# Optimization experiments

Hardware: AMD Instinct MI355X
Metric: run time of the kernel (lower is better)

## Reference

```python
import jax, jax.numpy as jnp
import numpy as np

P = 4; PSIZE = 16; EPS = 1e-8; LAM = 1e-3; MF = 2.0; ITERS = 2
BATCH = 64; A = 64; B = 8; C = 16; D = 16; E = 10


def _conv2d(x, w, b, stride, pad):
    y = jax.lax.conv_general_dilated(x, w, (stride, stride), [(pad, pad), (pad, pad)],
                                     dimension_numbers=('NCHW', 'OIHW', 'NCHW'))
    return y + b[None, :, None, None]


def _patches(x, K, stride):
    # x: (b, H, W, F) -> (b, oh, ow, K, K, F) sliding KxK windows with given stride
    b, H, W, F = x.shape
    oh = (H - K) // stride + 1
    ow = (W - K) // stride + 1
    ih = jnp.arange(oh) * stride
    iw = jnp.arange(ow) * stride
    p = x[:, ih[:, None] + jnp.arange(K)[None, :]]          # (b, oh, K, W, F)
    p = p[:, :, :, iw[:, None] + jnp.arange(K)[None, :]]    # (b, oh, K, ow, K, F)
    return p.transpose(0, 1, 3, 2, 4, 5), oh, ow


def _fuzzy_routing(v, a_in, beta_u, beta_a):
    # Fuzzy (c-means style) routing. v: (n, N, Cout, PSIZE) votes, a_in: (n, N).
    n, N, Cc, _ = v.shape
    r = jnp.full((n, N, Cc), 1.0 / Cc, dtype=v.dtype)
    aw = a_in[:, :, None]
    for t in range(ITERS):
        rm = (r ** MF) * aw                                             # fuzzified, activation-weighted
        coeff = rm / (jnp.sum(rm, axis=1, keepdims=True) + EPS)         # (n, N, C)
        mu = jnp.einsum('bnc,bncp->bcp', coeff, v)                      # (n, C, PSIZE)
        if t < ITERS - 1:
            dist = jnp.sum((v - mu[:, None]) ** 2, axis=-1) + EPS       # (n, N, C)
            inv = dist ** (-1.0 / (MF - 1.0))
            r = inv / (jnp.sum(inv, axis=2, keepdims=True) + EPS)
    sigma_sq = jnp.einsum('bnc,bncp->bcp', coeff, (v - mu[:, None]) ** 2) + EPS
    r_sum = jnp.sum((r ** MF) * aw, axis=1)                             # (n, C)
    cost = (beta_u[None, :, None] + 0.5 * jnp.log(sigma_sq)) * r_sum[:, :, None]
    a_out = jax.nn.sigmoid(LAM * (beta_a[None, :] - jnp.sum(cost, axis=2)))
    return mu, a_out


def _conv_caps(pose, a, W, beta_u, beta_a, K, stride):
    # pose: (b, H, W, Bi, PSIZE), a: (b, H, W, Bi); W: (K*K*Bi, Co, P, P)
    b, H, Wd, Bi, _ = pose.shape
    Co = W.shape[1]
    pp, oh, ow = _patches(pose.reshape(b, H, Wd, Bi * PSIZE), K, stride)
    ap, _, _ = _patches(a, K, stride)
    n = b * oh * ow
    pp = pp.reshape(n, K * K * Bi, P, P)
    ap = ap.reshape(n, K * K * Bi)
    v = jnp.einsum('nipq,icqr->nicpr', pp, W).reshape(n, K * K * Bi, Co, PSIZE)
    mu, a_out = _fuzzy_routing(v, ap, beta_u, beta_a)
    return mu.reshape(b, oh, ow, Co, PSIZE), a_out.reshape(b, oh, ow, Co)


def _class_caps(pose, a, W, beta_u, beta_a):
    # K=1, weight-shared over positions, with coordinate addition.
    b, H, Wd, Bi, _ = pose.shape
    Co = W.shape[1]
    v = jnp.einsum('bhwipq,icqr->bhwicpr', pose.reshape(b, H, Wd, Bi, P, P), W)
    v = v.reshape(b, H, Wd, Bi, Co, PSIZE)
    ch = (jnp.arange(H, dtype=v.dtype) / H)[None, :, None, None, None]
    cw = (jnp.arange(Wd, dtype=v.dtype) / Wd)[None, None, :, None, None]
    v = v.at[..., 0].add(ch)
    v = v.at[..., 1].add(cw)
    v = v.reshape(b, H * Wd * Bi, Co, PSIZE)
    return _fuzzy_routing(v, a.reshape(b, -1), beta_u, beta_a)


def setup_inputs():
    key = jax.random.key(0)
    ks = jax.random.split(key, 8)
    return {
        'x': jax.random.normal(ks[0], (BATCH, 1, 32, 32), jnp.float32),
        'conv1_w': jax.random.normal(ks[1], (A, 1, 5, 5), jnp.float32) * 0.1,
        'conv1_b': jnp.zeros((A,), jnp.float32),
        'bn_g': jnp.ones((A,), jnp.float32),
        'bn_b': jnp.zeros((A,), jnp.float32),
        'bn_mean': jnp.zeros((A,), jnp.float32),
        'bn_var': jnp.ones((A,), jnp.float32),
        'prim_pose_w': jax.random.normal(ks[2], (B * PSIZE, A, 1, 1), jnp.float32) * 0.1,
        'prim_pose_b': jnp.zeros((B * PSIZE,), jnp.float32),
        'prim_a_w': jax.random.normal(ks[3], (B, A, 1, 1), jnp.float32) * 0.1,
        'prim_a_b': jnp.zeros((B,), jnp.float32),
        'w1': jax.random.normal(ks[4], (3 * 3 * B, C, P, P), jnp.float32),
        'bu1': jnp.zeros((C,), jnp.float32),
        'ba1': jnp.zeros((C,), jnp.float32),
        'w2': jax.random.normal(ks[5], (3 * 3 * C, D, P, P), jnp.float32),
        'bu2': jnp.zeros((D,), jnp.float32),
        'ba2': jnp.zeros((D,), jnp.float32),
        'wc': jax.random.normal(ks[6], (D, E, P, P), jnp.float32),
        'buc': jnp.zeros((E,), jnp.float32),
        'bac': jnp.zeros((E,), jnp.float32),
    }


def reference(x, conv1_w, conv1_b, bn_g, bn_b, bn_mean, bn_var,
              prim_pose_w, prim_pose_b, prim_a_w, prim_a_b,
              w1, bu1, ba1, w2, bu2, ba2, wc, buc, bac):
    y = _conv2d(x, conv1_w, conv1_b, 2, 2)                               # (b, A, 16, 16)
    inv_std = jax.lax.rsqrt(bn_var + 1e-3)
    y = (y - bn_mean[None, :, None, None]) * (bn_g * inv_std)[None, :, None, None] + bn_b[None, :, None, None]
    y = jax.nn.relu(y)
    pose = _conv2d(y, prim_pose_w, prim_pose_b, 1, 0)                    # (b, B*16, 16, 16)
    a = jax.nn.sigmoid(_conv2d(y, prim_a_w, prim_a_b, 1, 0))             # (b, B, 16, 16)
    b_, _, H, Wd = a.shape
    pose = pose.transpose(0, 2, 3, 1).reshape(b_, H, Wd, B, PSIZE)
    a = a.transpose(0, 2, 3, 1)
    pose1, a1 = _conv_caps(pose, a, w1, bu1, ba1, 3, 2)
    pose2, a2 = _conv_caps(pose1, a1, w2, bu2, ba2, 3, 1)
    _, a_class = _class_caps(pose2, a2, wc, buc, bac)                    # (b, E)
    return a_class
```

## Files before the change

### kernel.cpp

```cpp
#include <hip/hip_runtime.h>
#include <math.h>

#define EPS_ 1e-8f
#define LAM_ 1e-3f

__global__ __launch_bounds__(256) void k_conv_bn(
    const float* __restrict__ x, const float* __restrict__ cw, const float* __restrict__ cb,
    const float* __restrict__ g, const float* __restrict__ bb,
    const float* __restrict__ mean, const float* __restrict__ var,
    float* __restrict__ y)
{
    int t = blockIdx.x * 256 + threadIdx.x;
    int ch = t & 63, w = (t >> 6) & 15, h = (t >> 10) & 15, b = t >> 14;
    const float* xb = x + b * 1024;
    const float* wc = cw + ch * 25;
    float acc = cb[ch];
    #pragma unroll
    for (int kh = 0; kh < 5; ++kh) {
        int ih = h * 2 - 2 + kh;
        if (ih < 0 || ih > 31) continue;
        #pragma unroll
        for (int kw = 0; kw < 5; ++kw) {
            int iw = w * 2 - 2 + kw;
            if (iw < 0 || iw > 31) continue;
            acc = fmaf(xb[ih * 32 + iw], wc[kh * 5 + kw], acc);
        }
    }
    float v = (acc - mean[ch]) * (g[ch] * rsqrtf(var[ch] + 1e-3f)) + bb[ch];
    y[t] = fmaxf(v, 0.f);
}

__global__ __launch_bounds__(256) void k_transw(
    const float* __restrict__ w1, const float* __restrict__ w2, const float* __restrict__ wc,
    const float* __restrict__ pw, const float* __restrict__ pb,
    const float* __restrict__ aw, const float* __restrict__ ab,
    float* __restrict__ w1t, float* __restrict__ w2t, float* __restrict__ wct,
    float* __restrict__ wpt)
{
    int t = blockIdx.x * 256 + threadIdx.x;
    if (t < 3616 * 16) {
        int m = t >> 4, e = t & 15, r = e >> 2, q = e & 3;
        const float* src; float* dst;
        if (m < 1152)      { src = w1 + m * 16;          dst = w1t + m * 16; }
        else if (m < 3456) { src = w2 + (m - 1152) * 16; dst = w2t + (m - 1152) * 16; }
        else               { src = wc + (m - 3456) * 16; dst = wct + (m - 3456) * 16; }
        dst[e] = src[q * 4 + r];
    } else if (t < 3616 * 16 + 65 * 136) {
        int idx = t - 3616 * 16;
        int o = idx % 136, j = idx / 136;
        float v;
        if (j == 64)       v = (o < 128) ? pb[o] : ab[o - 128];
        else if (o < 128)  v = pw[o * 64 + j];
        else               v = aw[(o - 128) * 64 + j];
        wpt[j * 136 + o] = v;
    }
}

__global__ __launch_bounds__(256) void k_prim(
    const float* __restrict__ y, const float* __restrict__ wpt,
    float* __restrict__ poseP, float* __restrict__ aP)
{
    int t = blockIdx.x * 256 + threadIdx.x;
    if (t >= 16384 * 34) return;
    int oq = t % 34;
    int pos = t / 34;
    const float* yp = y + pos * 64;
    float4 acc = *(const float4*)(wpt + 64 * 136 + oq * 4);
    #pragma unroll
    for (int j0 = 0; j0 < 64; j0 += 4) {
        float4 y4 = *(const float4*)(yp + j0);
        float4 w0 = *(const float4*)(wpt + (j0 + 0) * 136 + oq * 4);
        float4 w1 = *(const float4*)(wpt + (j0 + 1) * 136 + oq * 4);
        float4 w2 = *(const float4*)(wpt + (j0 + 2) * 136 + oq * 4);
        float4 w3 = *(const float4*)(wpt + (j0 + 3) * 136 + oq * 4);
        acc.x = fmaf(y4.x, w0.x, fmaf(y4.y, w1.x, fmaf(y4.z, w2.x, fmaf(y4.w, w3.x, acc.x))));
        acc.y = fmaf(y4.x, w0.y, fmaf(y4.y, w1.y, fmaf(y4.z, w2.y, fmaf(y4.w, w3.y, acc.y))));
        acc.z = fmaf(y4.x, w0.z, fmaf(y4.y, w1.z, fmaf(y4.z, w2.z, fmaf(y4.w, w3.z, acc.z))));
        acc.w = fmaf(y4.x, w0.w, fmaf(y4.y, w1.w, fmaf(y4.z, w2.w, fmaf(y4.w, w3.w, acc.w))));
    }
    if (oq < 32) {
        ((float4*)(poseP + pos * 128))[oq] = acc;
    } else {
        int oo = (oq - 32) * 4;
        float* ad = aP + pos * 8 + oo;
        ad[0] = 1.f / (1.f + __expf(-acc.x));
        ad[1] = 1.f / (1.f + __expf(-acc.y));
        ad[2] = 1.f / (1.f + __expf(-acc.z));
        ad[3] = 1.f / (1.f + __expf(-acc.w));
    }
}

template<int N, int C, int K, int S, int H, int W, int Bi, int OH, int OW>
__global__ __launch_bounds__(128) void k_caps_wave(
    const float* __restrict__ pose_in,
    const float* __restrict__ a_in,
    const float* __restrict__ Wt,
    const float* __restrict__ bu, const float* __restrict__ ba,
    float* __restrict__ pose_out,
    float* __restrict__ a_out)
{
    static_assert(C == 16 && N % 4 == 0, "");
    constexpr int NIT = N / 4;

    __shared__ __align__(16) float pp[2 * N * 16];
    __shared__ float ap[2 * N];

    const int t = threadIdx.x;
    const int w = t >> 6, lane = t & 63;
    float* ppw = pp + w * N * 16;
    float* apw = ap + w * N;

    const int n_ = blockIdx.x * 2 + w;
    const int b = n_ / (OH * OW);
    const int rem = n_ % (OH * OW);
    const int oh = rem / OW, ow = rem % OW;

    for (int idx = lane; idx < N * 4; idx += 64) {
        int i = idx >> 2, f = idx & 3;
        int bi = i % Bi;
        int k2 = i / Bi;
        int sw = ow * S + (k2 % K), sh = oh * S + (k2 / K);
        const float4* src = (const float4*)(pose_in + (((b * H + sh) * W + sw) * Bi + bi) * 16);
        ((float4*)(ppw + i * 16))[f] = src[f];
    }
    for (int i = lane; i < N; i += 64) {
        int bi = i % Bi;
        int k2 = i / Bi;
        int sw = ow * S + (k2 % K), sh = oh * S + (k2 / K);
        apw[i] = a_in[((b * H + sh) * W + sw) * Bi + bi];
    }
    __syncthreads();

    float suma = 0.f;
    for (int i = lane; i < N; i += 64) suma += apw[i];
    #pragma unroll
    for (int m = 1; m < 64; m <<= 1) suma += __shfl_xor(suma, m, 64);
    const float inv0 = __builtin_amdgcn_rcpf(suma + (float)(C * C) * EPS_);

    const int ig = t >> 4 & 3, cc = t & 15;

    float muU[16];
    #pragma unroll
    for (int e2 = 0; e2 < 16; ++e2) muU[e2] = 0.f;
    #pragma unroll 2
    for (int ii = 0; ii < NIT; ++ii) {
        int i = ig + ii * 4;
        const float4* pi4 = (const float4*)(ppw + i * 16);
        const float4* wt4 = (const float4*)(Wt + (i * C + cc) * 16);
        float4 pv[4] = { pi4[0], pi4[1], pi4[2], pi4[3] };
        float4 wv[4] = { wt4[0], wt4[1], wt4[2], wt4[3] };
        float co = apw[i] * inv0;
        #pragma unroll
        for (int e2 = 0; e2 < 16; ++e2) {
            float4 p4 = pv[e2 >> 2], w4 = wv[e2 & 3];
            float v = p4.x * w4.x + p4.y * w4.y + p4.z * w4.z + p4.w * w4.w;
            muU[e2] = fmaf(co, v, muU[e2]);
        }
    }
    #pragma unroll
    for (int e2 = 0; e2 < 16; ++e2) {
        muU[e2] += __shfl_xor(muU[e2], 16, 64);
        muU[e2] += __shfl_xor(muU[e2], 32, 64);
    }

    float SvU[16], Sv2U[16];
    #pragma unroll
    for (int e2 = 0; e2 < 16; ++e2) { SvU[e2] = 0.f; Sv2U[e2] = 0.f; }
    float rsum = 0.f;
    #pragma unroll 2
    for (int ii = 0; ii < NIT; ++ii) {
        int i = ig + ii * 4;
        const float4* pi4 = (const float4*)(ppw + i * 16);
        const float4* wt4 = (const float4*)(Wt + (i * C + cc) * 16);
        float4 pv[4] = { pi4[0], pi4[1], pi4[2], pi4[3] };
        float4 wv[4] = { wt4[0], wt4[1], wt4[2], wt4[3] };
        float vv[16];
        float dist = EPS_;
        #pragma unroll
        for (int e2 = 0; e2 < 16; ++e2) {
            float4 p4 = pv[e2 >> 2], w4 = wv[e2 & 3];
            float v = p4.x * w4.x + p4.y * w4.y + p4.z * w4.z + p4.w * w4.w;
            vv[e2] = v;
            float d = v - muU[e2];
            dist = fmaf(d, d, dist);
        }
        float inv = __builtin_amdgcn_rcpf(dist);
        float s = inv;
        #pragma unroll
        for (int m = 1; m < 16; m <<= 1) s += __shfl_xor(s, m, 64);
        float r1 = inv * __builtin_amdgcn_rcpf(s + EPS_);
        float rm = r1 * r1 * apw[i];
        rsum += rm;
        #pragma unroll
        for (int e2 = 0; e2 < 16; ++e2) {
            float rv = rm * vv[e2];
            SvU[e2] += rv;
            Sv2U[e2] = fmaf(rv, vv[e2], Sv2U[e2]);
        }
    }
    #pragma unroll
    for (int e2 = 0; e2 < 16; ++e2) {
        SvU[e2] += __shfl_xor(SvU[e2], 16, 64);
        SvU[e2] += __shfl_xor(SvU[e2], 32, 64);
        Sv2U[e2] += __shfl_xor(Sv2U[e2], 16, 64);
        Sv2U[e2] += __shfl_xor(Sv2U[e2], 32, 64);
    }
    rsum += __shfl_xor(rsum, 16, 64);
    rsum += __shfl_xor(rsum, 32, 64);

    const float id = 1.f / (rsum + EPS_);
    const float S0 = rsum * id;
    const float buc_ = bu[cc];
    float cs = 0.f;
    float4 outv[4];
    #pragma unroll
    for (int e2 = 0; e2 < 16; ++e2) {
        float Sv = SvU[e2] * id;
        float Sv2 = Sv2U[e2] * id;
        float sigma = fmaxf(Sv2 + Sv * Sv * (S0 - 2.f), 0.f) + EPS_;
        cs += (buc_ + 0.5f * __logf(sigma)) * rsum;
        ((float*)outv)[e2] = Sv;
    }
    if (lane < 16) {
        float4* pd = (float4*)(pose_out + (n_ * C + cc) * 16);
        pd[0] = outv[0]; pd[1] = outv[1]; pd[2] = outv[2]; pd[3] = outv[3];
        a_out[n_ * C + cc] = 1.f / (1.f + __expf(-(LAM_ * (ba[cc] - cs))));
    }
}

template<int N, int C, int H, int W, int Bi, int BLK>
__global__ __launch_bounds__(BLK) void k_caps_class(
    const float* __restrict__ pose_in, const float* __restrict__ a_in,
    const float* __restrict__ Wt,
    const float* __restrict__ bu, const float* __restrict__ ba,
    float* __restrict__ a_out)
{
    constexpr int NW  = BLK / 64;
    constexpr int NIG = BLK / 16;
    constexpr int NIT = (N + NIG - 1) / NIG;

    __shared__ __align__(16) float pp[N * 16];
    __shared__ float ap[N];
    __shared__ float coeff0[N];
    __shared__ float mu0[16 * 17];
    __shared__ float red1[NW * C * 17];
    __shared__ float red2[NW * C * 17];
    __shared__ float redr[NW * C];

    const int t = threadIdx.x;
    const int lane = t & 63;
    const int w = t >> 6;
    const int b = blockIdx.x;

    for (int idx = t; idx < N * 4; idx += BLK) {
        int i = idx >> 2, f = idx & 3;
        int bi = i % Bi;
        int hw = i / Bi;
        int sw = hw % W, sh = hw / W;
        const float4* src = (const float4*)(pose_in + (((b * H + sh) * W + sw) * Bi + bi) * 16);
        ((float4*)(pp + i * 16))[f] = src[f];
    }
    for (int i = t; i < N; i += BLK) {
        int bi = i % Bi;
        int hw = i / Bi;
        int sw = hw % W, sh = hw / W;
        ap[i] = a_in[((b * H + sh) * W + sw) * Bi + bi];
    }
    __syncthreads();

    {
        float part = 0.f;
        for (int i = t; i < N; i += BLK) part += ap[i];
        #pragma unroll
        for (int m = 1; m < 64; m <<= 1) part += __shfl_xor(part, m, 64);
        if (lane == 0) red1[w] = part;
        __syncthreads();
        float s = 0.f;
        #pragma unroll
        for (int ww = 0; ww < NW; ++ww) s += red1[ww];
        float inv0 = 1.f / (s + (float)(C * C) * EPS_);
        for (int i = t; i < N; i += BLK) coeff0[i] = ap[i] * inv0;
        __syncthreads();
    }

    const int ig = t >> 4, cc = t & 15;

    {
        float muU[16];
        #pragma unroll
        for (int e2 = 0; e2 < 16; ++e2) muU[e2] = 0.f;
        if (cc < C) {
            for (int ii = 0; ii < NIT; ++ii) {
                int i = ig + ii * NIG;
                if (i < N) {
                    const float4* pi4 = (const float4*)(pp + i * 16);
                    const float4* wt4 = (const float4*)(Wt + ((i % Bi) * C + cc) * 16);
                    float4 pv[4] = { pi4[0], pi4[1], pi4[2], pi4[3] };
                    float4 wv[4] = { wt4[0], wt4[1], wt4[2], wt4[3] };
                    float co = coeff0[i];
                    float chv = (float)(i / (W * Bi)) * (1.f / H);
                    float cwv = (float)((i / Bi) % W) * (1.f / W);
                    #pragma unroll
                    for (int e2 = 0; e2 < 16; ++e2) {
                        float4 p4 = pv[e2 >> 2], w4 = wv[e2 & 3];
                        float v = p4.x * w4.x + p4.y * w4.y + p4.z * w4.z + p4.w * w4.w;
                        if (e2 == 0) v += chv;
                        if (e2 == 1) v += cwv;
                        muU[e2] = fmaf(co, v, muU[e2]);
                    }
                }
            }
        }
        #pragma unroll
        for (int e2 = 0; e2 < 16; ++e2) {
            float xv = muU[e2];
            xv += __shfl_xor(xv, 16, 64);
            xv += __shfl_xor(xv, 32, 64);
            if (lane < 16 && lane < C) red1[(w * C + lane) * 17 + e2] = xv;
        }
        __syncthreads();
        if (t < 256) {
            int c = t >> 4, e = t & 15;
            if (c < C) {
                float m = 0.f;
                #pragma unroll
                for (int ww = 0; ww < NW; ++ww) m += red1[(ww * C + c) * 17 + e];
                mu0[c * 17 + e] = m;
            }
        }
        __syncthreads();
    }

    {
        float m0[16];
        if (cc < C) {
            #pragma unroll
            for (int e2 = 0; e2 < 16; ++e2) m0[e2] = mu0[cc * 17 + e2];
        }
        float SvU[16], Sv2U[16];
        #pragma unroll
        for (int e2 = 0; e2 < 16; ++e2) { SvU[e2] = 0.f; Sv2U[e2] = 0.f; }
        float rsumP = 0.f;

        for (int ii = 0; ii < NIT; ++ii) {
            int i = ig + ii * NIG;
            bool act = (i < N);
            float inv = 0.f;
            float vv[16];
            if (act && cc < C) {
                const float4* pi4 = (const float4*)(pp + i * 16);
                const float4* wt4 = (const float4*)(Wt + ((i % Bi) * C + cc) * 16);
                float4 pv[4] = { pi4[0], pi4[1], pi4[2], pi4[3] };
                float4 wv[4] = { wt4[0], wt4[1], wt4[2], wt4[3] };
                float chv = (float)(i / (W * Bi)) * (1.f / H);
                float cwv = (float)((i / Bi) % W) * (1.f / W);
                float dist = EPS_;
                #pragma unroll
                for (int e2 = 0; e2 < 16; ++e2) {
                    float4 p4 = pv[e2 >> 2], w4 = wv[e2 & 3];
                    float v = p4.x * w4.x + p4.y * w4.y + p4.z * w4.z + p4.w * w4.w;
                    if (e2 == 0) v += chv;
                    if (e2 == 1) v += cwv;
                    vv[e2] = v;
                    float d = v - m0[e2];
                    dist = fmaf(d, d, dist);
                }
                inv = 1.f / dist;
            }
            float s = inv;
            #pragma unroll
            for (int m = 1; m < 16; m <<= 1) s += __shfl_xor(s, m, 64);
            if (act && cc < C) {
                float r1 = inv / (s + EPS_);
                float rm = r1 * r1 * ap[i];
                rsumP += rm;
                #pragma unroll
                for (int e2 = 0; e2 < 16; ++e2) {
                    SvU[e2] = fmaf(rm, vv[e2], SvU[e2]);
                    Sv2U[e2] = fmaf(rm * vv[e2], vv[e2], Sv2U[e2]);
                }
            }
        }
        #pragma unroll
        for (int e2 = 0; e2 < 16; ++e2) {
            float xv = SvU[e2];
            xv += __shfl_xor(xv, 16, 64);
            xv += __shfl_xor(xv, 32, 64);
            float yv = Sv2U[e2];
            yv += __shfl_xor(yv, 16, 64);
            yv += __shfl_xor(yv, 32, 64);
            if (lane < 16 && lane < C) {
                red1[(w * C + lane) * 17 + e2] = xv;
                red2[(w * C + lane) * 17 + e2] = yv;
            }
        }
        {
            float rv = rsumP;
            rv += __shfl_xor(rv, 16, 64);
            rv += __shfl_xor(rv, 32, 64);
            if (lane < 16 && lane < C) redr[w * C + lane] = rv;
        }
        __syncthreads();
    }

    if (t < 256) {
        int c = t >> 4, e = t & 15;
        if (c < C) {
            float SvT = 0.f, Sv2T = 0.f, R = 0.f;
            #pragma unroll
            for (int ww = 0; ww < NW; ++ww) {
                SvT  += red1[(ww * C + c) * 17 + e];
                Sv2T += red2[(ww * C + c) * 17 + e];
                R    += redr[ww * C + c];
            }
            float id = 1.f / (R + EPS_);
            float S0 = R * id;
            float Sv = SvT * id;
            float Sv2 = Sv2T * id;
            float sigma = fmaxf(Sv2 + Sv * Sv * (S0 - 2.f), 0.f) + EPS_;
            float cost = (bu[c] + 0.5f * logf(sigma)) * R;
            float cs = cost;
            #pragma unroll
            for (int m = 1; m < 16; m <<= 1) cs += __shfl_xor(cs, m, 64);
            if (e == 0) a_out[b * C + c] = 1.f / (1.f + expf(-(LAM_ * (ba[c] - cs))));
        }
    }
}

extern "C" void kernel_launch(void* const* d_in, const int* in_sizes, int n_in,
                              void* d_out, int out_size, void* d_ws, size_t ws_size,
                              hipStream_t stream)
{
    const float* x   = (const float*)d_in[0];
    const float* c1w = (const float*)d_in[1];
    const float* c1b = (const float*)d_in[2];
    const float* bng = (const float*)d_in[3];
    const float* bnb = (const float*)d_in[4];
    const float* bnm = (const float*)d_in[5];
    const float* bnv = (const float*)d_in[6];
    const float* ppw = (const float*)d_in[7];
    const float* ppb = (const float*)d_in[8];
    const float* paw = (const float*)d_in[9];
    const float* pab = (const float*)d_in[10];
    const float* w1  = (const float*)d_in[11];
    const float* bu1 = (const float*)d_in[12];
    const float* ba1 = (const float*)d_in[13];
    const float* w2  = (const float*)d_in[14];
    const float* bu2 = (const float*)d_in[15];
    const float* ba2 = (const float*)d_in[16];
    const float* wcp = (const float*)d_in[17];
    const float* buc = (const float*)d_in[18];
    const float* bac = (const float*)d_in[19];
    float* out = (float*)d_out;

    float* ws    = (float*)d_ws;
    float* y     = ws;
    float* poseP = y + 1048576;
    float* aP    = poseP + 2097152;
    float* pose1 = aP + 131072;
    float* a1    = pose1 + 802816;
    float* pose2 = a1 + 50176;
    float* a2    = pose2 + 409600;
    float* w1t   = a2 + 25600;
    float* w2t   = w1t + 18432;
    float* wct   = w2t + 36864;
    float* wpt   = wct + 2560;

    hipLaunchKernelGGL(k_transw, dim3((3616 * 16 + 65 * 136 + 255) / 256), dim3(256), 0, stream,
                       w1, w2, wcp, ppw, ppb, paw, pab, w1t, w2t, wct, wpt);
    hipLaunchKernelGGL(k_conv_bn, dim3(4096), dim3(256), 0, stream,
                       x, c1w, c1b, bng, bnb, bnm, bnv, y);
    hipLaunchKernelGGL(k_prim, dim3((16384 * 34 + 255) / 256), dim3(256), 0, stream,
                       y, wpt, poseP, aP);
    hipLaunchKernelGGL((k_caps_wave<72, 16, 3, 2, 16, 16, 8, 7, 7>), dim3(1568), dim3(128), 0, stream,
                       poseP, aP, w1t, bu1, ba1, pose1, a1);
    hipLaunchKernelGGL((k_caps_wave<144, 16, 3, 1, 7, 7, 16, 5, 5>), dim3(800), dim3(128), 0, stream,
                       pose1, a1, w2t, bu2, ba2, pose2, a2);
    hipLaunchKernelGGL((k_caps_class<400, 10, 5, 5, 16, 1024>), dim3(64), dim3(1024), 0, stream,
                       pose2, a2, wct, buc, bac, out);
}
```

Measured before the change: 253.8 us.

## Split capsule routing per output position across multiple waves with LDS reductions

The conv-capsule routing kernel now assigns one output position per block and splits its input capsules across 2 or 4 waves, combining the partial mean and the weighted sums through shared-memory reductions between barriers. Before, each wave handled a whole position on its own. The aim is more parallelism and shorter serial per-wave loops on the latency-bound caps layers, at the cost of extra barriers and LDS traffic. The class-capsule kernel also switches several divides, log and exp calls to fast rcp and intrinsic approximations.

```diff
diff --git a/kernel.cpp b/kernel.cpp
--- a/kernel.cpp
+++ b/kernel.cpp
@@ -90,8 +90,8 @@
     }
 }
 
-template<int N, int C, int K, int S, int H, int W, int Bi, int OH, int OW>
-__global__ __launch_bounds__(128) void k_caps_wave(
+template<int N, int C, int K, int S, int H, int W, int Bi, int OH, int OW, int NW>
+__global__ __launch_bounds__(NW * 64) void k_caps_split(
     const float* __restrict__ pose_in,
     const float* __restrict__ a_in,
     const float* __restrict__ Wt,
@@ -99,57 +99,60 @@
     float* __restrict__ pose_out,
     float* __restrict__ a_out)
 {
-    static_assert(C == 16 && N % 4 == 0, "");
-    constexpr int NIT = N / 4;
-
-    __shared__ __align__(16) float pp[2 * N * 16];
-    __shared__ float ap[2 * N];
+    static_assert(C == 16 && N % (NW * 4) == 0, "");
+    constexpr int BLK = NW * 64;
+    constexpr int IW  = N / NW;
+    constexpr int NIT = IW / 4;
+
+    __shared__ __align__(16) float pp[N * 16];
+    __shared__ float ap[N];
+    __shared__ __align__(16) float red1[NW][16][20];
+    __shared__ __align__(16) float red2[NW][16][20];
+    __shared__ float redr[NW][16];
 
     const int t = threadIdx.x;
     const int w = t >> 6, lane = t & 63;
-    float* ppw = pp + w * N * 16;
-    float* apw = ap + w * N;
-
-    const int n_ = blockIdx.x * 2 + w;
+    const int n_ = blockIdx.x;
     const int b = n_ / (OH * OW);
     const int rem = n_ % (OH * OW);
     const int oh = rem / OW, ow = rem % OW;
 
-    for (int idx = lane; idx < N * 4; idx += 64) {
+    for (int idx = t; idx < N * 4; idx += BLK) {
         int i = idx >> 2, f = idx & 3;
         int bi = i % Bi;
         int k2 = i / Bi;
         int sw = ow * S + (k2 % K), sh = oh * S + (k2 / K);
         const float4* src = (const float4*)(pose_in + (((b * H + sh) * W + sw) * Bi + bi) * 16);
-        ((float4*)(ppw + i * 16))[f] = src[f];
-    }
-    for (int i = lane; i < N; i += 64) {
+        ((float4*)(pp + i * 16))[f] = src[f];
+    }
+    for (int i = t; i < N; i += BLK) {
         int bi = i % Bi;
         int k2 = i / Bi;
         int sw = ow * S + (k2 % K), sh = oh * S + (k2 / K);
-        apw[i] = a_in[((b * H + sh) * W + sw) * Bi + bi];
+        ap[i] = a_in[((b * H + sh) * W + sw) * Bi + bi];
     }
     __syncthreads();
 
     float suma = 0.f;
-    for (int i = lane; i < N; i += 64) suma += apw[i];
+    for (int i = lane; i < N; i += 64) suma += ap[i];
     #pragma unroll
     for (int m = 1; m < 64; m <<= 1) suma += __shfl_xor(suma, m, 64);
     const float inv0 = __builtin_amdgcn_rcpf(suma + (float)(C * C) * EPS_);
 
-    const int ig = t >> 4 & 3, cc = t & 15;
+    const int ig = (lane >> 4) & 3, cc = lane & 15;
+    const int ibase = w * IW;
 
     float muU[16];
     #pragma unroll
     for (int e2 = 0; e2 < 16; ++e2) muU[e2] = 0.f;
     #pragma unroll 2
     for (int ii = 0; ii < NIT; ++ii) {
-        int i = ig + ii * 4;
-        const float4* pi4 = (const float4*)(ppw + i * 16);
+        int i = ibase + ig + ii * 4;
+        const float4* pi4 = (const float4*)(pp + i * 16);
         const float4* wt4 = (const float4*)(Wt + (i * C + cc) * 16);
         float4 pv[4] = { pi4[0], pi4[1], pi4[2], pi4[3] };
         float4 wv[4] = { wt4[0], wt4[1], wt4[2], wt4[3] };
-        float co = apw[i] * inv0;
+        float co = ap[i] * inv0;
         #pragma unroll
         for (int e2 = 0; e2 < 16; ++e2) {
             float4 p4 = pv[e2 >> 2], w4 = wv[e2 & 3];
@@ -162,6 +165,29 @@
         muU[e2] += __shfl_xor(muU[e2], 16, 64);
         muU[e2] += __shfl_xor(muU[e2], 32, 64);
     }
+    if (lane < 16) {
+        float4* dst = (float4*)&red1[w][lane][0];
+        dst[0] = *(float4*)&muU[0];
+        dst[1] = *(float4*)&muU[4];
+        dst[2] = *(float4*)&muU[8];
+        dst[3] = *(float4*)&muU[12];
+    }
+    __syncthreads();
+
+    float m0[16];
+    {
+        #pragma unroll
+        for (int f = 0; f < 4; ++f) {
+            float4 s = *(const float4*)&red1[0][cc][f * 4];
+            #pragma unroll
+            for (int ww = 1; ww < NW; ++ww) {
+                float4 p = *(const float4*)&red1[ww][cc][f * 4];
+                s.x += p.x; s.y += p.y; s.z += p.z; s.w += p.w;
+            }
+            *(float4*)&m0[f * 4] = s;
+        }
+    }
+    __syncthreads();
 
     float SvU[16], Sv2U[16];
     #pragma unroll
@@ -169,8 +195,8 @@
     float rsum = 0.f;
     #pragma unroll 2
     for (int ii = 0; ii < NIT; ++ii) {
-        int i = ig + ii * 4;
-        const float4* pi4 = (const float4*)(ppw + i * 16);
+        int i = ibase + ig + ii * 4;
+        const float4* pi4 = (const float4*)(pp + i * 16);
         const float4* wt4 = (const float4*)(Wt + (i * C + cc) * 16);
         float4 pv[4] = { pi4[0], pi4[1], pi4[2], pi4[3] };
         float4 wv[4] = { wt4[0], wt4[1], wt4[2], wt4[3] };
@@ -181,7 +207,7 @@
             float4 p4 = pv[e2 >> 2], w4 = wv[e2 & 3];
             float v = p4.x * w4.x + p4.y * w4.y + p4.z * w4.z + p4.w * w4.w;
             vv[e2] = v;
-            float d = v - muU[e2];
+            float d = v - m0[e2];
             dist = fmaf(d, d, dist);
         }
         float inv = __builtin_amdgcn_rcpf(dist);
@@ -189,7 +215,7 @@
         #pragma unroll
         for (int m = 1; m < 16; m <<= 1) s += __shfl_xor(s, m, 64);
         float r1 = inv * __builtin_amdgcn_rcpf(s + EPS_);
-        float rm = r1 * r1 * apw[i];
+        float rm = r1 * r1 * ap[i];
         rsum += rm;
         #pragma unroll
         for (int e2 = 0; e2 < 16; ++e2) {
@@ -207,24 +233,55 @@
     }
     rsum += __shfl_xor(rsum, 16, 64);
     rsum += __shfl_xor(rsum, 32, 64);
-
-    const float id = 1.f / (rsum + EPS_);
-    const float S0 = rsum * id;
-    const float buc_ = bu[cc];
-    float cs = 0.f;
-    float4 outv[4];
-    #pragma unroll
-    for (int e2 = 0; e2 < 16; ++e2) {
-        float Sv = SvU[e2] * id;
-        float Sv2 = Sv2U[e2] * id;
-        float sigma = fmaxf(Sv2 + Sv * Sv * (S0 - 2.f), 0.f) + EPS_;
-        cs += (buc_ + 0.5f * __logf(sigma)) * rsum;
-        ((float*)outv)[e2] = Sv;
-    }
     if (lane < 16) {
-        float4* pd = (float4*)(pose_out + (n_ * C + cc) * 16);
-        pd[0] = outv[0]; pd[1] = outv[1]; pd[2] = outv[2]; pd[3] = outv[3];
-        a_out[n_ * C + cc] = 1.f / (1.f + __expf(-(LAM_ * (ba[cc] - cs))));
+        float4* d1 = (float4*)&red1[w][lane][0];
+        float4* d2 = (float4*)&red2[w][lane][0];
+        d1[0] = *(float4*)&SvU[0];  d1[1] = *(float4*)&SvU[4];
+        d1[2] = *(float4*)&SvU[8];  d1[3] = *(float4*)&SvU[12];
+        d2[0] = *(float4*)&Sv2U[0]; d2[1] = *(float4*)&Sv2U[4];
+        d2[2] = *(float4*)&Sv2U[8]; d2[3] = *(float4*)&Sv2U[12];
+        redr[w][lane] = rsum;
+    }
+    __syncthreads();
+
+    if (w == 0) {
+        float SvT[16], Sv2T[16];
+        #pragma unroll
+        for (int f = 0; f < 4; ++f) {
+            float4 s1 = *(const float4*)&red1[0][cc][f * 4];
+            float4 s2 = *(const float4*)&red2[0][cc][f * 4];
+            #pragma unroll
+            for (int ww = 1; ww < NW; ++ww) {
+                float4 p1 = *(const float4*)&red1[ww][cc][f * 4];
+                float4 p2 = *(const float4*)&red2[ww][cc][f * 4];
+                s1.x += p1.x; s1.y += p1.y; s1.z += p1.z; s1.w += p1.w;
+                s2.x += p2.x; s2.y += p2.y; s2.z += p2.z; s2.w += p2.w;
+            }
+            *(float4*)&SvT[f * 4] = s1;
+            *(float4*)&Sv2T[f * 4] = s2;
+        }
+        float R = 0.f;
+        #pragma unroll
+        for (int ww = 0; ww < NW; ++ww) R += redr[ww][cc];
+
+        const float id = 1.f / (R + EPS_);
+        const float S0 = R * id;
+        const float buc_ = bu[cc];
+        float cs = 0.f;
+        float4 outv[4];
+        #pragma unroll
+        for (int e2 = 0; e2 < 16; ++e2) {
+            float Sv = SvT[e2] * id;
+            float Sv2 = Sv2T[e2] * id;
+            float sigma = fmaxf(Sv2 + Sv * Sv * (S0 - 2.f), 0.f) + EPS_;
+            cs += (buc_ + 0.5f * __logf(sigma)) * R;
+            ((float*)outv)[e2] = Sv;
+        }
+        if (lane < 16) {
+            float4* pd = (float4*)(pose_out + (n_ * C + cc) * 16);
+            pd[0] = outv[0]; pd[1] = outv[1]; pd[2] = outv[2]; pd[3] = outv[3];
+            a_out[n_ * C + cc] = 1.f / (1.f + __expf(-(LAM_ * (ba[cc] - cs))));
+        }
     }
 }
 
@@ -278,7 +335,7 @@
         float s = 0.f;
         #pragma unroll
         for (int ww = 0; ww < NW; ++ww) s += red1[ww];
-        float inv0 = 1.f / (s + (float)(C * C) * EPS_);
+        float inv0 = __builtin_amdgcn_rcpf(s + (float)(C * C) * EPS_);
         for (int i = t; i < N; i += BLK) coeff0[i] = ap[i] * inv0;
         __syncthreads();
     }
@@ -365,13 +422,13 @@
                     float d = v - m0[e2];
                     dist = fmaf(d, d, dist);
                 }
-                inv = 1.f / dist;
+                inv = __builtin_amdgcn_rcpf(dist);
             }
             float s = inv;
             #pragma unroll
             for (int m = 1; m < 16; m <<= 1) s += __shfl_xor(s, m, 64);
             if (act && cc < C) {
-                float r1 = inv / (s + EPS_);
+                float r1 = inv * __builtin_amdgcn_rcpf(s + EPS_);
                 float rm = r1 * r1 * ap[i];
                 rsumP += rm;
                 #pragma unroll
@@ -418,11 +475,11 @@
             float Sv = SvT * id;
             float Sv2 = Sv2T * id;
             float sigma = fmaxf(Sv2 + Sv * Sv * (S0 - 2.f), 0.f) + EPS_;
-            float cost = (bu[c] + 0.5f * logf(sigma)) * R;
+            float cost = (bu[c] + 0.5f * __logf(sigma)) * R;
             float cs = cost;
             #pragma unroll
             for (int m = 1; m < 16; m <<= 1) cs += __shfl_xor(cs, m, 64);
-            if (e == 0) a_out[b * C + c] = 1.f / (1.f + expf(-(LAM_ * (ba[c] - cs))));
+            if (e == 0) a_out[b * C + c] = 1.f / (1.f + __expf(-(LAM_ * (ba[c] - cs))));
         }
     }
 }
@@ -472,9 +529,9 @@
                        x, c1w, c1b, bng, bnb, bnm, bnv, y);
     hipLaunchKernelGGL(k_prim, dim3((16384 * 34 + 255) / 256), dim3(256), 0, stream,
                        y, wpt, poseP, aP);
-    hipLaunchKernelGGL((k_caps_wave<72, 16, 3, 2, 16, 16, 8, 7, 7>), dim3(1568), dim3(128), 0, stream,
+    hipLaunchKernelGGL((k_caps_split<72, 16, 3, 2, 16, 16, 8, 7, 7, 2>), dim3(3136), dim3(128), 0, stream,
                        poseP, aP, w1t, bu1, ba1, pose1, a1);
-    hipLaunchKernelGGL((k_caps_wave<144, 16, 3, 1, 7, 7, 16, 5, 5>), dim3(800), dim3(128), 0, stream,
+    hipLaunchKernelGGL((k_caps_split<144, 16, 3, 1, 7, 7, 16, 5, 5, 4>), dim3(1600), dim3(256), 0, stream,
                        pose1, a1, w2t, bu2, ba2, pose2, a2);
     hipLaunchKernelGGL((k_caps_class<400, 10, 5, 5, 16, 1024>), dim3(64), dim3(1024), 0, stream,
                        pose2, a2, wct, buc, bac, out);
```

After: 263.1 us. 1.04x slower.
